# Optimization experiments

Measured on AMD Instinct MI355X. Metric: run time of the kernel, lower is better.

## Reference

```python
import jax, jax.numpy as jnp
import numpy as np

H = 12
DK = 64


def setup_inputs() -> dict:
    key = jax.random.key(0)
    ks = jax.random.split(key, 6)
    bs, ne, d = 32, 20, H * DK
    R = jax.random.normal(ks[0], (bs, ne, ne, d), dtype=jnp.float32)
    R_mas = jax.random.randint(ks[1], (bs, ne, ne, 1), 0, 2).astype(jnp.float32)
    WQ_w = jax.random.normal(ks[2], (DK, DK), dtype=jnp.float32) * (1.0 / np.sqrt(DK))
    WK_w = jax.random.normal(ks[3], (DK, DK), dtype=jnp.float32) * (1.0 / np.sqrt(DK))
    WV_w = jax.random.normal(ks[4], (DK, DK), dtype=jnp.float32) * (1.0 / np.sqrt(DK))
    zb = jnp.zeros((DK,), dtype=jnp.float32)
    return {"R": R, "R_mas": R_mas, "WQ_w": WQ_w, "WQ_b": zb, "WK_w": WK_w,
            "WK_b": zb, "WV_w": WV_w, "WV_b": zb}


def reference(R, R_mas, WQ_w, WQ_b, WK_w, WK_b, WV_w, WV_b):
    bs, ne, _, d = R.shape
    h, dk = H, DK
    n = ne * ne
    # (bs, h, ne, ne, dk)
    Rh = R.reshape(bs, ne, ne, h, dk).transpose(0, 3, 1, 2, 4)
    # per-head QKV linears (torch Linear: y = x @ W.T + b)
    Q = (Rh @ WQ_w.T + WQ_b).reshape(bs, h, n, dk)
    K = (Rh @ WK_w.T + WK_b).reshape(bs, h, n, dk)
    V = (Rh @ WV_w.T + WV_b).reshape(bs, h, n, dk)
    mas = R_mas.reshape(bs, 1, n)                      # (bs,1,n)
    att_mas = mas[:, :, :, None] * mas[:, :, None, :]  # (bs,1,n,n)
    alpha = jnp.einsum('bhqd,bhkd->bhqk', Q, K)        # (bs,h,n,n)
    alpha = alpha - (1.0 - att_mas) * 100000.0         # mask BEFORE scaling (faithful)
    alpha = jax.nn.softmax(alpha / jnp.sqrt(jnp.float32(dk)), axis=-1)
    R_Z = jnp.einsum('bhqk,bhkd->bhqd', alpha, V).reshape(bs, h, ne, ne, dk)
    R_Z = R_Z * R_mas.reshape(bs, 1, ne, ne, 1)
    # (bs, ne, ne, h*dk)
    return R_Z.transpose(0, 2, 3, 1, 4).reshape(bs, ne, ne, h * dk)
```

## Files before the change

### kernel.cpp

```cpp
#include <hip/hip_runtime.h>

typedef float    f32x4 __attribute__((ext_vector_type(4)));
typedef _Float16 f16x8 __attribute__((ext_vector_type(8)));
typedef _Float16 f16x4 __attribute__((ext_vector_type(4)));
typedef _Float16 f16x2 __attribute__((ext_vector_type(2)));
typedef __fp16   fp16x2_raw __attribute__((ext_vector_type(2)));

#define MFMA16 __builtin_amdgcn_mfma_f32_16x16x32_f16

__device__ __forceinline__ f16x2 pkrtz(float a, float b) {
    fp16x2_raw t = __builtin_amdgcn_cvt_pkrtz(a, b);
    union { fp16x2_raw r; f16x2 h; } u;
    u.r = t;
    return u.h;
}
#define PKRTZ pkrtz

#define NQ     400
#define DMODEL 768

#define SCL 0.18033688011112042f
#define PEN 18033.688011112043f
#define M0  8.0f

#define K_OFF    0
#define VT_OFF   51200
#define W_OFF    105472
#define PEN_OFF  130048
#define BIAS_OFF 131648
#define MKB_OFF  132416
#define SMEM_BYTES 132480

__device__ __forceinline__ f16x8 cvt8(const float* rp) {
    f32x4 u0 = *(const f32x4*)(rp);
    f32x4 u1 = *(const f32x4*)(rp + 4);
    union { f16x2 h2[4]; f16x8 v; } u;
    u.h2[0] = PKRTZ(u0[0], u0[1]);
    u.h2[1] = PKRTZ(u0[2], u0[3]);
    u.h2[2] = PKRTZ(u1[0], u1[1]);
    u.h2[3] = PKRTZ(u1[2], u1[3]);
    return u.v;
}

__device__ __forceinline__ void proj_v(char* smem, f16x8 af0, f16x8 af1,
                                       int t, int g, int q16, int csw) {
    #pragma unroll
    for (int cg = 0; cg < 4; ++cg) {
        const int col = cg * 16 + q16;
        const float bb = *(const float*)(smem + BIAS_OFF + (128 + col) * 4);
        f32x4 acc = {bb, bb, bb, bb};
        f16x8 wb0 = *(const f16x8*)(smem + W_OFF + 16384 + col * 128 + ((g * 16) ^ csw));
        f16x8 wb1 = *(const f16x8*)(smem + W_OFF + 16384 + col * 128 + ((64 + g * 16) ^ csw));
        acc = MFMA16(af0, wb0, acc, 0, 0, 0);
        acc = MFMA16(af1, wb1, acc, 0, 0, 0);
        union { f16x2 h2[2]; f16x4 v; } hv;
        hv.h2[0] = PKRTZ(acc[0], acc[1]);
        hv.h2[1] = PKRTZ(acc[2], acc[3]);
        *(f16x4*)(smem + VT_OFF + col * 848 + (t >> 1) * 64 + g * 16 + (t & 1) * 8) = hv.v;
    }
}

__device__ __forceinline__ void proj_k(char* smem, f16x8 af0, f16x8 af1,
                                       int kk, int g, int q16, int csw) {
    #pragma unroll
    for (int cg = 0; cg < 4; ++cg) {
        const int d0 = cg * 16 + 4 * g;
        f32x4 acc = *(const f32x4*)(smem + BIAS_OFF + (64 + d0) * 4);
        f16x8 wb0 = *(const f16x8*)(smem + W_OFF + 8192 + (cg * 16 + q16) * 128 + ((g * 16) ^ csw));
        f16x8 wb1 = *(const f16x8*)(smem + W_OFF + 8192 + (cg * 16 + q16) * 128 + ((64 + g * 16) ^ csw));
        acc = MFMA16(wb0, af0, acc, 0, 0, 0);
        acc = MFMA16(wb1, af1, acc, 0, 0, 0);
        union { f16x2 h2[2]; f16x4 v; } hv;
        hv.h2[0] = PKRTZ(acc[0], acc[1]);
        hv.h2[1] = PKRTZ(acc[2], acc[3]);
        const int pos2 = ((cg & 2) << 5) + g * 16 + (cg & 1) * 8;
        *(f16x4*)(smem + K_OFF + kk * 128 + (pos2 ^ csw)) = hv.v;
    }
}

__device__ __forceinline__ void proj_q(char* smem, f16x8 af0, f16x8 af1,
                                       int g, int q16, int csw, f16x8 (&qreg)[2]) {
    f32x4 qa[4];
    #pragma unroll
    for (int cg = 0; cg < 4; ++cg) {
        const int d0 = cg * 16 + 4 * g;
        f32x4 acc = *(const f32x4*)(smem + BIAS_OFF + d0 * 4);
        f16x8 wb0 = *(const f16x8*)(smem + W_OFF + (cg * 16 + q16) * 128 + ((g * 16) ^ csw));
        f16x8 wb1 = *(const f16x8*)(smem + W_OFF + (cg * 16 + q16) * 128 + ((64 + g * 16) ^ csw));
        acc = MFMA16(wb0, af0, acc, 0, 0, 0);
        acc = MFMA16(wb1, af1, acc, 0, 0, 0);
        qa[cg] = acc;
    }
    union { f16x2 h2[4]; f16x8 v; } u0, u1;
    u0.h2[0] = PKRTZ(qa[0][0], qa[0][1]);
    u0.h2[1] = PKRTZ(qa[0][2], qa[0][3]);
    u0.h2[2] = PKRTZ(qa[1][0], qa[1][1]);
    u0.h2[3] = PKRTZ(qa[1][2], qa[1][3]);
    u1.h2[0] = PKRTZ(qa[2][0], qa[2][1]);
    u1.h2[1] = PKRTZ(qa[2][2], qa[2][3]);
    u1.h2[2] = PKRTZ(qa[3][0], qa[3][1]);
    u1.h2[3] = PKRTZ(qa[3][2], qa[3][3]);
    qreg[0] = u0.v;
    qreg[1] = u1.v;
}

__global__ __launch_bounds__(1024, 4)
void attn_fused(const float* __restrict__ R, const float* __restrict__ Rmas,
                const float* __restrict__ Wq, const float* __restrict__ bq,
                const float* __restrict__ Wk, const float* __restrict__ bk,
                const float* __restrict__ Wv, const float* __restrict__ bv,
                float* __restrict__ out)
{
    extern __shared__ char smem[];
    const int tid  = threadIdx.x;
    const int lane = tid & 63;
    const int wv   = tid >> 6;
    const int g    = lane >> 4;
    const int q16  = lane & 15;
    const int csw  = (q16 & 7) << 4;

    const int blk = blockIdx.x;
    const int b   = blk / 12;
    const int h   = blk % 12;

    {
        if (tid < 768) {
            const int m   = tid >> 8;
            const int idx = tid & 255;
            const int row = idx >> 2;
            const int c0  = (idx & 3) << 4;
            const float* Wm = (m == 0 ? Wq : (m == 1 ? Wk : Wv)) + row * 64 + c0;
            const int sw = (row & 7) << 4;
            #pragma unroll
            for (int k2 = 0; k2 < 2; ++k2) {
                f32x4 v0 = *(const f32x4*)(Wm + 8 * k2);
                f32x4 v1 = *(const f32x4*)(Wm + 8 * k2 + 4);
                union { f16x2 h2[4]; f16x8 v; } hv;
                hv.h2[0] = PKRTZ(v0[0], v0[1]);
                hv.h2[1] = PKRTZ(v0[2], v0[3]);
                hv.h2[2] = PKRTZ(v1[0], v1[1]);
                hv.h2[3] = PKRTZ(v1[2], v1[3]);
                *(f16x8*)(smem + W_OFF + m * 8192 + row * 128 + ((c0 * 2 + 16 * k2) ^ sw)) = hv.v;
            }
        } else if (tid < 960) {
            const int j = tid - 768;
            const float* bms[3] = {bq, bk, bv};
            *(float*)(smem + BIAS_OFF + j * 4) = bms[j >> 6][j & 63];
        }
        if (wv < 7) {
            const int i = (wv << 6) | lane;
            const float mval = (i < NQ) ? Rmas[b * NQ + i] : 0.0f;
            unsigned long long bb = __ballot(mval != 0.0f);
            if (lane == 0) {
                ((unsigned*)(smem + MKB_OFF))[2 * wv]     = (unsigned)bb;
                ((unsigned*)(smem + MKB_OFF))[2 * wv + 1] = (unsigned)(bb >> 32);
            }
        }
        if (tid < 256) {
            const int r = tid >> 2, c = tid & 3;
            *(f16x4*)(smem + VT_OFF + r * 848 + 768 + c * 16 + 8) = (f16x4){0, 0, 0, 0};
        }
    }
    __syncthreads();

    const float* Rbh = R + (size_t)b * NQ * DMODEL + h * 64;

    f16x8 qreg0[2], qreg1[2];
    int qt0 = -1, qt1 = -1;
    #pragma unroll
    for (int i = 0; i < 2; ++i) {
        const int t = wv + 16 * i;
        if (t < 25) {
            const float* rp = Rbh + (size_t)(t * 16 + q16) * DMODEL + g * 8;
            f16x8 af0 = cvt8(rp);
            f16x8 af1 = cvt8(rp + 32);
            proj_k(smem, af0, af1, t * 16 + q16, g, q16, csw);
            proj_v(smem, af0, af1, t, g, q16, csw);
        }
    }
    {
        const int t0 = 2 * wv;
        if (t0 < 25) {
            const float* rp = Rbh + (size_t)(t0 * 16 + q16) * DMODEL + g * 8;
            f16x8 af0 = cvt8(rp);
            f16x8 af1 = cvt8(rp + 32);
            proj_q(smem, af0, af1, g, q16, csw, qreg0);
            qt0 = t0;
        }
        const int t1 = 2 * wv + 1;
        if (t1 < 25) {
            const float* rp = Rbh + (size_t)(t1 * 16 + q16) * DMODEL + g * 8;
            f16x8 af0 = cvt8(rp);
            f16x8 af1 = cvt8(rp + 32);
            proj_q(smem, af0, af1, g, q16, csw, qreg1);
            qt1 = t1;
        }
    }
    if (wv == 15) {
        #pragma unroll
        for (int i = 0; i < 7; ++i) {
            const int k = i * 64 + lane;
            if (k < NQ) {
                const unsigned bit =
                    (((const unsigned*)(smem + MKB_OFF))[k >> 5] >> (k & 31)) & 1u;
                *(float*)(smem + PEN_OFF + k * 4) = bit ? -M0 : -(M0 + PEN);
            }
        }
    }
    __syncthreads();

    if (qt0 >= 0) {
        const bool has2 = (qt1 >= 0);
        const int qrow0 = qt0 * 16 + q16;
        const unsigned qb0 = (((const unsigned*)(smem + MKB_OFF))[qrow0 >> 5] >> (qrow0 & 31)) & 1u;
        const int qrow1 = (has2 ? qt1 : qt0) * 16 + q16;
        const unsigned qb1 = (((const unsigned*)(smem + MKB_OFF))[qrow1 >> 5] >> (qrow1 & 31)) & 1u;

        const int kbase = K_OFF + q16 * 128;
        const int o0 = (g * 16) ^ csw;
        const int o1 = (64 + g * 16) ^ csw;

        f32x4 oc0[4], oc1[4];
        #pragma unroll
        for (int cg = 0; cg < 4; ++cg) {
            oc0[cg] = (f32x4){0.f, 0.f, 0.f, 0.f};
            oc1[cg] = (f32x4){0.f, 0.f, 0.f, 0.f};
        }
        float ps0 = 0.f, ps1 = 0.f;

        f16x8 ka0 = *(const f16x8*)(smem + kbase + o0);
        f16x8 ka1 = *(const f16x8*)(smem + kbase + o1);
        f16x8 kb0 = *(const f16x8*)(smem + kbase + 2048 + o0);
        f16x8 kb1 = *(const f16x8*)(smem + kbase + 2048 + o1);

        #pragma unroll 1
        for (int kc = 0; kc < 12; ++kc) {
            f32x4 pa4 = *(const f32x4*)(smem + PEN_OFF + (kc * 32 + 4 * g) * 4);
            f32x4 pb4 = *(const f32x4*)(smem + PEN_OFF + (kc * 32 + 16 + 4 * g) * 4);

            __builtin_amdgcn_s_setprio(1);
            f32x4 accA0 = {0.f, 0.f, 0.f, 0.f};
            accA0 = MFMA16(ka0, qreg0[0], accA0, 0, 0, 0);
            accA0 = MFMA16(ka1, qreg0[1], accA0, 0, 0, 0);
            f32x4 accB0 = {0.f, 0.f, 0.f, 0.f};
            accB0 = MFMA16(kb0, qreg0[0], accB0, 0, 0, 0);
            accB0 = MFMA16(kb1, qreg0[1], accB0, 0, 0, 0);
            f32x4 accA1 = {0.f, 0.f, 0.f, 0.f};
            f32x4 accB1 = {0.f, 0.f, 0.f, 0.f};
            if (has2) {
                accA1 = MFMA16(ka0, qreg1[0], accA1, 0, 0, 0);
                accA1 = MFMA16(ka1, qreg1[1], accA1, 0, 0, 0);
                accB1 = MFMA16(kb0, qreg1[0], accB1, 0, 0, 0);
                accB1 = MFMA16(kb1, qreg1[1], accB1, 0, 0, 0);
            }
            __builtin_amdgcn_s_setprio(0);

            const char* kn = smem + kbase + (kc + 1) * 4096;
            ka0 = *(const f16x8*)(kn + o0);
            ka1 = *(const f16x8*)(kn + o1);
            kb0 = *(const f16x8*)(kn + 2048 + o0);
            kb1 = *(const f16x8*)(kn + 2048 + o1);

            const float e0 = __builtin_amdgcn_exp2f(fmaf(accA0[0], SCL, pa4[0]));
            const float e1 = __builtin_amdgcn_exp2f(fmaf(accA0[1], SCL, pa4[1]));
            const float e2 = __builtin_amdgcn_exp2f(fmaf(accA0[2], SCL, pa4[2]));
            const float e3 = __builtin_amdgcn_exp2f(fmaf(accA0[3], SCL, pa4[3]));
            const float e4 = __builtin_amdgcn_exp2f(fmaf(accB0[0], SCL, pb4[0]));
            const float e5 = __builtin_amdgcn_exp2f(fmaf(accB0[1], SCL, pb4[1]));
            const float e6 = __builtin_amdgcn_exp2f(fmaf(accB0[2], SCL, pb4[2]));
            const float e7 = __builtin_amdgcn_exp2f(fmaf(accB0[3], SCL, pb4[3]));
            ps0 += ((e0 + e1) + (e2 + e3)) + ((e4 + e5) + (e6 + e7));
            union { f16x2 h2[4]; f16x8 v; } pu0;
            pu0.h2[0] = PKRTZ(e0, e1);
            pu0.h2[1] = PKRTZ(e2, e3);
            pu0.h2[2] = PKRTZ(e4, e5);
            pu0.h2[3] = PKRTZ(e6, e7);
            const f16x8 pfrag0 = pu0.v;

            f16x8 pfrag1;
            if (has2) {
                const float f0 = __builtin_amdgcn_exp2f(fmaf(accA1[0], SCL, pa4[0]));
                const float f1 = __builtin_amdgcn_exp2f(fmaf(accA1[1], SCL, pa4[1]));
                const float f2 = __builtin_amdgcn_exp2f(fmaf(accA1[2], SCL, pa4[2]));
                const float f3 = __builtin_amdgcn_exp2f(fmaf(accA1[3], SCL, pa4[3]));
                const float f4 = __builtin_amdgcn_exp2f(fmaf(accB1[0], SCL, pb4[0]));
                const float f5 = __builtin_amdgcn_exp2f(fmaf(accB1[1], SCL, pb4[1]));
                const float f6 = __builtin_amdgcn_exp2f(fmaf(accB1[2], SCL, pb4[2]));
                const float f7 = __builtin_amdgcn_exp2f(fmaf(accB1[3], SCL, pb4[3]));
                ps1 += ((f0 + f1) + (f2 + f3)) + ((f4 + f5) + (f6 + f7));
                union { f16x2 h2[4]; f16x8 v; } pu1;
                pu1.h2[0] = PKRTZ(f0, f1);
                pu1.h2[1] = PKRTZ(f2, f3);
                pu1.h2[2] = PKRTZ(f4, f5);
                pu1.h2[3] = PKRTZ(f6, f7);
                pfrag1 = pu1.v;
            }

            __builtin_amdgcn_s_setprio(1);
            #pragma unroll
            for (int cg = 0; cg < 4; ++cg) {
                f16x8 vb = *(const f16x8*)(smem + VT_OFF + (cg * 16 + q16) * 848 + kc * 64 + g * 16);
                oc0[cg] = MFMA16(pfrag0, vb, oc0[cg], 0, 0, 0);
                if (has2) oc1[cg] = MFMA16(pfrag1, vb, oc1[cg], 0, 0, 0);
            }
            __builtin_amdgcn_s_setprio(0);
        }
        {
            f32x4 pa4 = *(const f32x4*)(smem + PEN_OFF + (384 + 4 * g) * 4);
            f32x4 accA0 = {0.f, 0.f, 0.f, 0.f};
            accA0 = MFMA16(ka0, qreg0[0], accA0, 0, 0, 0);
            accA0 = MFMA16(ka1, qreg0[1], accA0, 0, 0, 0);
            const float e0 = __builtin_amdgcn_exp2f(fmaf(accA0[0], SCL, pa4[0]));
            const float e1 = __builtin_amdgcn_exp2f(fmaf(accA0[1], SCL, pa4[1]));
            const float e2 = __builtin_amdgcn_exp2f(fmaf(accA0[2], SCL, pa4[2]));
            const float e3 = __builtin_amdgcn_exp2f(fmaf(accA0[3], SCL, pa4[3]));
            ps0 += (e0 + e1) + (e2 + e3);
            union { f16x2 h2[4]; f16x8 v; } pu0;
            pu0.h2[0] = PKRTZ(e0, e1);
            pu0.h2[1] = PKRTZ(e2, e3);
            pu0.h2[2] = (f16x2){0, 0};
            pu0.h2[3] = (f16x2){0, 0};
            const f16x8 pfrag0 = pu0.v;

            f16x8 pfrag1;
            if (has2) {
                f32x4 accA1 = {0.f, 0.f, 0.f, 0.f};
                accA1 = MFMA16(ka0, qreg1[0], accA1, 0, 0, 0);
                accA1 = MFMA16(ka1, qreg1[1], accA1, 0, 0, 0);
                const float f0 = __builtin_amdgcn_exp2f(fmaf(accA1[0], SCL, pa4[0]));
                const float f1 = __builtin_amdgcn_exp2f(fmaf(accA1[1], SCL, pa4[1]));
                const float f2 = __builtin_amdgcn_exp2f(fmaf(accA1[2], SCL, pa4[2]));
                const float f3 = __builtin_amdgcn_exp2f(fmaf(accA1[3], SCL, pa4[3]));
                ps1 += (f0 + f1) + (f2 + f3);
                union { f16x2 h2[4]; f16x8 v; } pu1;
                pu1.h2[0] = PKRTZ(f0, f1);
                pu1.h2[1] = PKRTZ(f2, f3);
                pu1.h2[2] = (f16x2){0, 0};
                pu1.h2[3] = (f16x2){0, 0};
                pfrag1 = pu1.v;
            }
            #pragma unroll
            for (int cg = 0; cg < 4; ++cg) {
                f16x8 vb = *(const f16x8*)(smem + VT_OFF + (cg * 16 + q16) * 848 + 12 * 64 + g * 16);
                oc0[cg] = MFMA16(pfrag0, vb, oc0[cg], 0, 0, 0);
                if (has2) oc1[cg] = MFMA16(pfrag1, vb, oc1[cg], 0, 0, 0);
            }
        }

        ps0 += __shfl_xor(ps0, 16);
        ps0 += __shfl_xor(ps0, 32);
        const float myrs0 = qb0 ? __builtin_amdgcn_rcpf(ps0) : 0.0f;
        float rs[4];
        #pragma unroll
        for (int r = 0; r < 4; ++r) rs[r] = __shfl(myrs0, 4 * g + r);
        float* op0 = out + (size_t)(b * NQ + qt0 * 16) * DMODEL + h * 64;
        #pragma unroll
        for (int r = 0; r < 4; ++r) {
            #pragma unroll
            for (int cg = 0; cg < 4; ++cg)
                op0[(4 * g + r) * DMODEL + cg * 16 + q16] = oc0[cg][r] * rs[r];
        }
        if (has2) {
            ps1 += __shfl_xor(ps1, 16);
            ps1 += __shfl_xor(ps1, 32);
            const float myrs1 = qb1 ? __builtin_amdgcn_rcpf(ps1) : 0.0f;
            #pragma unroll
            for (int r = 0; r < 4; ++r) rs[r] = __shfl(myrs1, 4 * g + r);
            float* op1 = out + (size_t)(b * NQ + qt1 * 16) * DMODEL + h * 64;
            #pragma unroll
            for (int r = 0; r < 4; ++r) {
                #pragma unroll
                for (int cg = 0; cg < 4; ++cg)
                    op1[(4 * g + r) * DMODEL + cg * 16 + q16] = oc1[cg][r] * rs[r];
            }
        }
    }
}

extern "C" void kernel_launch(void* const* d_in, const int* in_sizes, int n_in,
                              void* d_out, int out_size, void* d_ws, size_t ws_size,
                              hipStream_t stream) {
    const float* R    = (const float*)d_in[0];
    const float* Rmas = (const float*)d_in[1];
    const float* Wq   = (const float*)d_in[2];
    const float* bq   = (const float*)d_in[3];
    const float* Wk   = (const float*)d_in[4];
    const float* bk   = (const float*)d_in[5];
    const float* Wv   = (const float*)d_in[6];
    const float* bv   = (const float*)d_in[7];
    float* out = (float*)d_out;

    (void)hipFuncSetAttribute(reinterpret_cast<const void*>(attn_fused),
                              hipFuncAttributeMaxDynamicSharedMemorySize, SMEM_BYTES);
    attn_fused<<<dim3(384), dim3(1024), SMEM_BYTES, stream>>>(R, Rmas, Wq, bq, Wk, bk, Wv, bv, out);
}
```

Baseline: 45.26 us.

## Rebalance grid to 256 blocks, each doing one full head plus half a head

The kernel now launches 256 blocks (8 per batch) instead of 384 (one per batch-head). Each block processes one full head and then half of a second head's query tiles, reusing the shared weights and mask setup. The aim is to match the block count to the GPU's 256 compute units so there is no partial second wave. The cost is that K/V projection for the split heads is recomputed by both blocks that share them, plus an extra barrier between the two segments.

```diff
diff --git a/kernel.cpp b/kernel.cpp
--- a/kernel.cpp
+++ b/kernel.cpp
@@ -120,8 +120,11 @@
     const int csw  = (q16 & 7) << 4;
 
     const int blk = blockIdx.x;
-    const int b   = blk / 12;
-    const int h   = blk % 12;
+    const int b   = blk >> 3;
+    const int j   = blk & 7;
+    int h_full, h_half, qlo2, nt2;
+    if (j & 1) { h_half = (3 * j - 1) >> 1; qlo2 = 13; nt2 = 12; h_full = (3 * j + 1) >> 1; }
+    else       { h_full = (3 * j) >> 1;     h_half = h_full + 1; qlo2 = 0;  nt2 = 13; }
 
     {
         if (tid < 768) {
@@ -143,9 +146,9 @@
                 *(f16x8*)(smem + W_OFF + m * 8192 + row * 128 + ((c0 * 2 + 16 * k2) ^ sw)) = hv.v;
             }
         } else if (tid < 960) {
-            const int j = tid - 768;
+            const int jj = tid - 768;
             const float* bms[3] = {bq, bk, bv};
-            *(float*)(smem + BIAS_OFF + j * 4) = bms[j >> 6][j & 63];
+            *(float*)(smem + BIAS_OFF + jj * 4) = bms[jj >> 6][jj & 63];
         }
         if (wv < 7) {
             const int i = (wv << 6) | lane;
@@ -163,215 +166,224 @@
     }
     __syncthreads();
 
-    const float* Rbh = R + (size_t)b * NQ * DMODEL + h * 64;
-
-    f16x8 qreg0[2], qreg1[2];
-    int qt0 = -1, qt1 = -1;
-    #pragma unroll
-    for (int i = 0; i < 2; ++i) {
-        const int t = wv + 16 * i;
-        if (t < 25) {
+    #pragma unroll 1
+    for (int seg = 0; seg < 2; ++seg) {
+        const int h   = seg ? h_half : h_full;
+        const int qlo = seg ? qlo2 : 0;
+        const int nt  = seg ? nt2  : 25;
+        const float* Rbh = R + (size_t)b * NQ * DMODEL + h * 64;
+
+        if (seg) __syncthreads();
+
+        f16x8 qreg0[2], qreg1[2];
+        const int qt0 = (wv < nt)      ? (qlo + wv)      : -1;
+        const int qt1 = (wv + 16 < nt) ? (qlo + wv + 16) : -1;
+        {
+            const int t = wv;
             const float* rp = Rbh + (size_t)(t * 16 + q16) * DMODEL + g * 8;
             f16x8 af0 = cvt8(rp);
             f16x8 af1 = cvt8(rp + 32);
             proj_k(smem, af0, af1, t * 16 + q16, g, q16, csw);
             proj_v(smem, af0, af1, t, g, q16, csw);
-        }
-    }
-    {
-        const int t0 = 2 * wv;
-        if (t0 < 25) {
-            const float* rp = Rbh + (size_t)(t0 * 16 + q16) * DMODEL + g * 8;
+            if (qt0 == t) proj_q(smem, af0, af1, g, q16, csw, qreg0);
+        }
+        if (wv >= 7) {
+            const int t = wv + 9;
+            const float* rp = Rbh + (size_t)(t * 16 + q16) * DMODEL + g * 8;
+            f16x8 af0 = cvt8(rp);
+            f16x8 af1 = cvt8(rp + 32);
+            proj_k(smem, af0, af1, t * 16 + q16, g, q16, csw);
+            proj_v(smem, af0, af1, t, g, q16, csw);
+        }
+        if (qt0 >= 0 && qt0 != wv) {
+            const float* rp = Rbh + (size_t)(qt0 * 16 + q16) * DMODEL + g * 8;
             f16x8 af0 = cvt8(rp);
             f16x8 af1 = cvt8(rp + 32);
             proj_q(smem, af0, af1, g, q16, csw, qreg0);
-            qt0 = t0;
-        }
-        const int t1 = 2 * wv + 1;
-        if (t1 < 25) {
-            const float* rp = Rbh + (size_t)(t1 * 16 + q16) * DMODEL + g * 8;
+        }
+        if (qt1 >= 0) {
+            const float* rp = Rbh + (size_t)(qt1 * 16 + q16) * DMODEL + g * 8;
             f16x8 af0 = cvt8(rp);
             f16x8 af1 = cvt8(rp + 32);
             proj_q(smem, af0, af1, g, q16, csw, qreg1);
-            qt1 = t1;
-        }
-    }
-    if (wv == 15) {
-        #pragma unroll
-        for (int i = 0; i < 7; ++i) {
-            const int k = i * 64 + lane;
-            if (k < NQ) {
-                const unsigned bit =
-                    (((const unsigned*)(smem + MKB_OFF))[k >> 5] >> (k & 31)) & 1u;
-                *(float*)(smem + PEN_OFF + k * 4) = bit ? -M0 : -(M0 + PEN);
-            }
-        }
-    }
-    __syncthreads();
-
-    if (qt0 >= 0) {
-        const bool has2 = (qt1 >= 0);
-        const int qrow0 = qt0 * 16 + q16;
-        const unsigned qb0 = (((const unsigned*)(smem + MKB_OFF))[qrow0 >> 5] >> (qrow0 & 31)) & 1u;
-        const int qrow1 = (has2 ? qt1 : qt0) * 16 + q16;
-        const unsigned qb1 = (((const unsigned*)(smem + MKB_OFF))[qrow1 >> 5] >> (qrow1 & 31)) & 1u;
-
-        const int kbase = K_OFF + q16 * 128;
-        const int o0 = (g * 16) ^ csw;
-        const int o1 = (64 + g * 16) ^ csw;
-
-        f32x4 oc0[4], oc1[4];
-        #pragma unroll
-        for (int cg = 0; cg < 4; ++cg) {
-            oc0[cg] = (f32x4){0.f, 0.f, 0.f, 0.f};
-            oc1[cg] = (f32x4){0.f, 0.f, 0.f, 0.f};
-        }
-        float ps0 = 0.f, ps1 = 0.f;
-
-        f16x8 ka0 = *(const f16x8*)(smem + kbase + o0);
-        f16x8 ka1 = *(const f16x8*)(smem + kbase + o1);
-        f16x8 kb0 = *(const f16x8*)(smem + kbase + 2048 + o0);
-        f16x8 kb1 = *(const f16x8*)(smem + kbase + 2048 + o1);
-
-        #pragma unroll 1
-        for (int kc = 0; kc < 12; ++kc) {
-            f32x4 pa4 = *(const f32x4*)(smem + PEN_OFF + (kc * 32 + 4 * g) * 4);
-            f32x4 pb4 = *(const f32x4*)(smem + PEN_OFF + (kc * 32 + 16 + 4 * g) * 4);
-
-            __builtin_amdgcn_s_setprio(1);
-            f32x4 accA0 = {0.f, 0.f, 0.f, 0.f};
-            accA0 = MFMA16(ka0, qreg0[0], accA0, 0, 0, 0);
-            accA0 = MFMA16(ka1, qreg0[1], accA0, 0, 0, 0);
-            f32x4 accB0 = {0.f, 0.f, 0.f, 0.f};
-            accB0 = MFMA16(kb0, qreg0[0], accB0, 0, 0, 0);
-            accB0 = MFMA16(kb1, qreg0[1], accB0, 0, 0, 0);
-            f32x4 accA1 = {0.f, 0.f, 0.f, 0.f};
-            f32x4 accB1 = {0.f, 0.f, 0.f, 0.f};
-            if (has2) {
-                accA1 = MFMA16(ka0, qreg1[0], accA1, 0, 0, 0);
-                accA1 = MFMA16(ka1, qreg1[1], accA1, 0, 0, 0);
-                accB1 = MFMA16(kb0, qreg1[0], accB1, 0, 0, 0);
-                accB1 = MFMA16(kb1, qreg1[1], accB1, 0, 0, 0);
-            }
-            __builtin_amdgcn_s_setprio(0);
-
-            const char* kn = smem + kbase + (kc + 1) * 4096;
-            ka0 = *(const f16x8*)(kn + o0);
-            ka1 = *(const f16x8*)(kn + o1);
-            kb0 = *(const f16x8*)(kn + 2048 + o0);
-            kb1 = *(const f16x8*)(kn + 2048 + o1);
-
-            const float e0 = __builtin_amdgcn_exp2f(fmaf(accA0[0], SCL, pa4[0]));
-            const float e1 = __builtin_amdgcn_exp2f(fmaf(accA0[1], SCL, pa4[1]));
-            const float e2 = __builtin_amdgcn_exp2f(fmaf(accA0[2], SCL, pa4[2]));
-            const float e3 = __builtin_amdgcn_exp2f(fmaf(accA0[3], SCL, pa4[3]));
-            const float e4 = __builtin_amdgcn_exp2f(fmaf(accB0[0], SCL, pb4[0]));
-            const float e5 = __builtin_amdgcn_exp2f(fmaf(accB0[1], SCL, pb4[1]));
-            const float e6 = __builtin_amdgcn_exp2f(fmaf(accB0[2], SCL, pb4[2]));
-            const float e7 = __builtin_amdgcn_exp2f(fmaf(accB0[3], SCL, pb4[3]));
-            ps0 += ((e0 + e1) + (e2 + e3)) + ((e4 + e5) + (e6 + e7));
-            union { f16x2 h2[4]; f16x8 v; } pu0;
-            pu0.h2[0] = PKRTZ(e0, e1);
-            pu0.h2[1] = PKRTZ(e2, e3);
-            pu0.h2[2] = PKRTZ(e4, e5);
-            pu0.h2[3] = PKRTZ(e6, e7);
-            const f16x8 pfrag0 = pu0.v;
-
-            f16x8 pfrag1;
-            if (has2) {
-                const float f0 = __builtin_amdgcn_exp2f(fmaf(accA1[0], SCL, pa4[0]));
-                const float f1 = __builtin_amdgcn_exp2f(fmaf(accA1[1], SCL, pa4[1]));
-                const float f2 = __builtin_amdgcn_exp2f(fmaf(accA1[2], SCL, pa4[2]));
-                const float f3 = __builtin_amdgcn_exp2f(fmaf(accA1[3], SCL, pa4[3]));
-                const float f4 = __builtin_amdgcn_exp2f(fmaf(accB1[0], SCL, pb4[0]));
-                const float f5 = __builtin_amdgcn_exp2f(fmaf(accB1[1], SCL, pb4[1]));
-                const float f6 = __builtin_amdgcn_exp2f(fmaf(accB1[2], SCL, pb4[2]));
-                const float f7 = __builtin_amdgcn_exp2f(fmaf(accB1[3], SCL, pb4[3]));
-                ps1 += ((f0 + f1) + (f2 + f3)) + ((f4 + f5) + (f6 + f7));
-                union { f16x2 h2[4]; f16x8 v; } pu1;
-                pu1.h2[0] = PKRTZ(f0, f1);
-                pu1.h2[1] = PKRTZ(f2, f3);
-                pu1.h2[2] = PKRTZ(f4, f5);
-                pu1.h2[3] = PKRTZ(f6, f7);
-                pfrag1 = pu1.v;
-            }
-
-            __builtin_amdgcn_s_setprio(1);
+        }
+        if (seg == 0 && wv == 15) {
+            #pragma unroll
+            for (int i = 0; i < 7; ++i) {
+                const int k = i * 64 + lane;
+                if (k < NQ) {
+                    const unsigned bit =
+                        (((const unsigned*)(smem + MKB_OFF))[k >> 5] >> (k & 31)) & 1u;
+                    *(float*)(smem + PEN_OFF + k * 4) = bit ? -M0 : -(M0 + PEN);
+                }
+            }
+        }
+        __syncthreads();
+
+        if (qt0 >= 0) {
+            const bool has2 = (qt1 >= 0);
+            const int qrow0 = qt0 * 16 + q16;
+            const unsigned qb0 = (((const unsigned*)(smem + MKB_OFF))[qrow0 >> 5] >> (qrow0 & 31)) & 1u;
+            const int qrow1 = (has2 ? qt1 : qt0) * 16 + q16;
+            const unsigned qb1 = (((const unsigned*)(smem + MKB_OFF))[qrow1 >> 5] >> (qrow1 & 31)) & 1u;
+
+            const int kbase = K_OFF + q16 * 128;
+            const int o0 = (g * 16) ^ csw;
+            const int o1 = (64 + g * 16) ^ csw;
+
+            f32x4 oc0[4], oc1[4];
             #pragma unroll
             for (int cg = 0; cg < 4; ++cg) {
-                f16x8 vb = *(const f16x8*)(smem + VT_OFF + (cg * 16 + q16) * 848 + kc * 64 + g * 16);
-                oc0[cg] = MFMA16(pfrag0, vb, oc0[cg], 0, 0, 0);
-                if (has2) oc1[cg] = MFMA16(pfrag1, vb, oc1[cg], 0, 0, 0);
-            }
-            __builtin_amdgcn_s_setprio(0);
-        }
-        {
-            f32x4 pa4 = *(const f32x4*)(smem + PEN_OFF + (384 + 4 * g) * 4);
-            f32x4 accA0 = {0.f, 0.f, 0.f, 0.f};
-            accA0 = MFMA16(ka0, qreg0[0], accA0, 0, 0, 0);
-            accA0 = MFMA16(ka1, qreg0[1], accA0, 0, 0, 0);
-            const float e0 = __builtin_amdgcn_exp2f(fmaf(accA0[0], SCL, pa4[0]));
-            const float e1 = __builtin_amdgcn_exp2f(fmaf(accA0[1], SCL, pa4[1]));
-            const float e2 = __builtin_amdgcn_exp2f(fmaf(accA0[2], SCL, pa4[2]));
-            const float e3 = __builtin_amdgcn_exp2f(fmaf(accA0[3], SCL, pa4[3]));
-            ps0 += (e0 + e1) + (e2 + e3);
-            union { f16x2 h2[4]; f16x8 v; } pu0;
-            pu0.h2[0] = PKRTZ(e0, e1);
-            pu0.h2[1] = PKRTZ(e2, e3);
-            pu0.h2[2] = (f16x2){0, 0};
-            pu0.h2[3] = (f16x2){0, 0};
-            const f16x8 pfrag0 = pu0.v;
-
-            f16x8 pfrag1;
-            if (has2) {
+                oc0[cg] = (f32x4){0.f, 0.f, 0.f, 0.f};
+                oc1[cg] = (f32x4){0.f, 0.f, 0.f, 0.f};
+            }
+            float ps0 = 0.f, ps1 = 0.f;
+
+            f16x8 ka0 = *(const f16x8*)(smem + kbase + o0);
+            f16x8 ka1 = *(const f16x8*)(smem + kbase + o1);
+            f16x8 kb0 = *(const f16x8*)(smem + kbase + 2048 + o0);
+            f16x8 kb1 = *(const f16x8*)(smem + kbase + 2048 + o1);
+
+            #pragma unroll 1
+            for (int kc = 0; kc < 12; ++kc) {
+                f32x4 pa4 = *(const f32x4*)(smem + PEN_OFF + (kc * 32 + 4 * g) * 4);
+                f32x4 pb4 = *(const f32x4*)(smem + PEN_OFF + (kc * 32 + 16 + 4 * g) * 4);
+
+                __builtin_amdgcn_s_setprio(1);
+                f32x4 accA0 = {0.f, 0.f, 0.f, 0.f};
+                accA0 = MFMA16(ka0, qreg0[0], accA0, 0, 0, 0);
+                accA0 = MFMA16(ka1, qreg0[1], accA0, 0, 0, 0);
+                f32x4 accB0 = {0.f, 0.f, 0.f, 0.f};
+                accB0 = MFMA16(kb0, qreg0[0], accB0, 0, 0, 0);
+                accB0 = MFMA16(kb1, qreg0[1], accB0, 0, 0, 0);
                 f32x4 accA1 = {0.f, 0.f, 0.f, 0.f};
-                accA1 = MFMA16(ka0, qreg1[0], accA1, 0, 0, 0);
-                accA1 = MFMA16(ka1, qreg1[1], accA1, 0, 0, 0);
-                const float f0 = __builtin_amdgcn_exp2f(fmaf(accA1[0], SCL, pa4[0]));
-                const float f1 = __builtin_amdgcn_exp2f(fmaf(accA1[1], SCL, pa4[1]));
-                const float f2 = __builtin_amdgcn_exp2f(fmaf(accA1[2], SCL, pa4[2]));
-                const float f3 = __builtin_amdgcn_exp2f(fmaf(accA1[3], SCL, pa4[3]));
-                ps1 += (f0 + f1) + (f2 + f3);
-                union { f16x2 h2[4]; f16x8 v; } pu1;
-                pu1.h2[0] = PKRTZ(f0, f1);
-                pu1.h2[1] = PKRTZ(f2, f3);
-                pu1.h2[2] = (f16x2){0, 0};
-                pu1.h2[3] = (f16x2){0, 0};
-                pfrag1 = pu1.v;
-            }
+                f32x4 accB1 = {0.f, 0.f, 0.f, 0.f};
+                if (has2) {
+                    accA1 = MFMA16(ka0, qreg1[0], accA1, 0, 0, 0);
+                    accA1 = MFMA16(ka1, qreg1[1], accA1, 0, 0, 0);
+                    accB1 = MFMA16(kb0, qreg1[0], accB1, 0, 0, 0);
+                    accB1 = MFMA16(kb1, qreg1[1], accB1, 0, 0, 0);
+                }
+                __builtin_amdgcn_s_setprio(0);
+
+                const char* kn = smem + kbase + (kc + 1) * 4096;
+                ka0 = *(const f16x8*)(kn + o0);
+                ka1 = *(const f16x8*)(kn + o1);
+                kb0 = *(const f16x8*)(kn + 2048 + o0);
+                kb1 = *(const f16x8*)(kn + 2048 + o1);
+
+                const float e0 = __builtin_amdgcn_exp2f(fmaf(accA0[0], SCL, pa4[0]));
+                const float e1 = __builtin_amdgcn_exp2f(fmaf(accA0[1], SCL, pa4[1]));
+                const float e2 = __builtin_amdgcn_exp2f(fmaf(accA0[2], SCL, pa4[2]));
+                const float e3 = __builtin_amdgcn_exp2f(fmaf(accA0[3], SCL, pa4[3]));
+                const float e4 = __builtin_amdgcn_exp2f(fmaf(accB0[0], SCL, pb4[0]));
+                const float e5 = __builtin_amdgcn_exp2f(fmaf(accB0[1], SCL, pb4[1]));
+                const float e6 = __builtin_amdgcn_exp2f(fmaf(accB0[2], SCL, pb4[2]));
+                const float e7 = __builtin_amdgcn_exp2f(fmaf(accB0[3], SCL, pb4[3]));
+                ps0 += ((e0 + e1) + (e2 + e3)) + ((e4 + e5) + (e6 + e7));
+                union { f16x2 h2[4]; f16x8 v; } pu0;
+                pu0.h2[0] = PKRTZ(e0, e1);
+                pu0.h2[1] = PKRTZ(e2, e3);
+                pu0.h2[2] = PKRTZ(e4, e5);
+                pu0.h2[3] = PKRTZ(e6, e7);
+                const f16x8 pfrag0 = pu0.v;
+
+                f16x8 pfrag1;
+                if (has2) {
+                    const float f0 = __builtin_amdgcn_exp2f(fmaf(accA1[0], SCL, pa4[0]));
+                    const float f1 = __builtin_amdgcn_exp2f(fmaf(accA1[1], SCL, pa4[1]));
+                    const float f2 = __builtin_amdgcn_exp2f(fmaf(accA1[2], SCL, pa4[2]));
+                    const float f3 = __builtin_amdgcn_exp2f(fmaf(accA1[3], SCL, pa4[3]));
+                    const float f4 = __builtin_amdgcn_exp2f(fmaf(accB1[0], SCL, pb4[0]));
+                    const float f5 = __builtin_amdgcn_exp2f(fmaf(accB1[1], SCL, pb4[1]));
+                    const float f6 = __builtin_amdgcn_exp2f(fmaf(accB1[2], SCL, pb4[2]));
+                    const float f7 = __builtin_amdgcn_exp2f(fmaf(accB1[3], SCL, pb4[3]));
+                    ps1 += ((f0 + f1) + (f2 + f3)) + ((f4 + f5) + (f6 + f7));
+                    union { f16x2 h2[4]; f16x8 v; } pu1;
+                    pu1.h2[0] = PKRTZ(f0, f1);
+                    pu1.h2[1] = PKRTZ(f2, f3);
+                    pu1.h2[2] = PKRTZ(f4, f5);
+                    pu1.h2[3] = PKRTZ(f6, f7);
+                    pfrag1 = pu1.v;
+                }
+
+                __builtin_amdgcn_s_setprio(1);
+                #pragma unroll
+                for (int cg = 0; cg < 4; ++cg) {
+                    f16x8 vb = *(const f16x8*)(smem + VT_OFF + (cg * 16 + q16) * 848 + kc * 64 + g * 16);
+                    oc0[cg] = MFMA16(pfrag0, vb, oc0[cg], 0, 0, 0);
+                    if (has2) oc1[cg] = MFMA16(pfrag1, vb, oc1[cg], 0, 0, 0);
+                }
+                __builtin_amdgcn_s_setprio(0);
+            }
+            {
+                f32x4 pa4 = *(const f32x4*)(smem + PEN_OFF + (384 + 4 * g) * 4);
+                f32x4 accA0 = {0.f, 0.f, 0.f, 0.f};
+                accA0 = MFMA16(ka0, qreg0[0], accA0, 0, 0, 0);
+                accA0 = MFMA16(ka1, qreg0[1], accA0, 0, 0, 0);
+                const float e0 = __builtin_amdgcn_exp2f(fmaf(accA0[0], SCL, pa4[0]));
+                const float e1 = __builtin_amdgcn_exp2f(fmaf(accA0[1], SCL, pa4[1]));
+                const float e2 = __builtin_amdgcn_exp2f(fmaf(accA0[2], SCL, pa4[2]));
+                const float e3 = __builtin_amdgcn_exp2f(fmaf(accA0[3], SCL, pa4[3]));
+                ps0 += (e0 + e1) + (e2 + e3);
+                union { f16x2 h2[4]; f16x8 v; } pu0;
+                pu0.h2[0] = PKRTZ(e0, e1);
+                pu0.h2[1] = PKRTZ(e2, e3);
+                pu0.h2[2] = (f16x2){0, 0};
+                pu0.h2[3] = (f16x2){0, 0};
+                const f16x8 pfrag0 = pu0.v;
+
+                f16x8 pfrag1;
+                if (has2) {
+                    f32x4 accA1 = {0.f, 0.f, 0.f, 0.f};
+                    accA1 = MFMA16(ka0, qreg1[0], accA1, 0, 0, 0);
+                    accA1 = MFMA16(ka1, qreg1[1], accA1, 0, 0, 0);
+                    const float f0 = __builtin_amdgcn_exp2f(fmaf(accA1[0], SCL, pa4[0]));
+                    const float f1 = __builtin_amdgcn_exp2f(fmaf(accA1[1], SCL, pa4[1]));
+                    const float f2 = __builtin_amdgcn_exp2f(fmaf(accA1[2], SCL, pa4[2]));
+                    const float f3 = __builtin_amdgcn_exp2f(fmaf(accA1[3], SCL, pa4[3]));
+                    ps1 += (f0 + f1) + (f2 + f3);
+                    union { f16x2 h2[4]; f16x8 v; } pu1;
+                    pu1.h2[0] = PKRTZ(f0, f1);
+                    pu1.h2[1] = PKRTZ(f2, f3);
+                    pu1.h2[2] = (f16x2){0, 0};
+                    pu1.h2[3] = (f16x2){0, 0};
+                    pfrag1 = pu1.v;
+                }
+                #pragma unroll
+                for (int cg = 0; cg < 4; ++cg) {
+                    f16x8 vb = *(const f16x8*)(smem + VT_OFF + (cg * 16 + q16) * 848 + 12 * 64 + g * 16);
+                    oc0[cg] = MFMA16(pfrag0, vb, oc0[cg], 0, 0, 0);
+                    if (has2) oc1[cg] = MFMA16(pfrag1, vb, oc1[cg], 0, 0, 0);
+                }
+            }
+
+            ps0 += __shfl_xor(ps0, 16);
+            ps0 += __shfl_xor(ps0, 32);
+            const float myrs0 = qb0 ? __builtin_amdgcn_rcpf(ps0) : 0.0f;
+            float rs[4];
             #pragma unroll
-            for (int cg = 0; cg < 4; ++cg) {
-                f16x8 vb = *(const f16x8*)(smem + VT_OFF + (cg * 16 + q16) * 848 + 12 * 64 + g * 16);
-                oc0[cg] = MFMA16(pfrag0, vb, oc0[cg], 0, 0, 0);
-                if (has2) oc1[cg] = MFMA16(pfrag1, vb, oc1[cg], 0, 0, 0);
-            }
-        }
-
-        ps0 += __shfl_xor(ps0, 16);
-        ps0 += __shfl_xor(ps0, 32);
-        const float myrs0 = qb0 ? __builtin_amdgcn_rcpf(ps0) : 0.0f;
-        float rs[4];
-        #pragma unroll
-        for (int r = 0; r < 4; ++r) rs[r] = __shfl(myrs0, 4 * g + r);
-        float* op0 = out + (size_t)(b * NQ + qt0 * 16) * DMODEL + h * 64;
-        #pragma unroll
-        for (int r = 0; r < 4; ++r) {
-            #pragma unroll
-            for (int cg = 0; cg < 4; ++cg)
-                op0[(4 * g + r) * DMODEL + cg * 16 + q16] = oc0[cg][r] * rs[r];
-        }
-        if (has2) {
-            ps1 += __shfl_xor(ps1, 16);
-            ps1 += __shfl_xor(ps1, 32);
-            const float myrs1 = qb1 ? __builtin_amdgcn_rcpf(ps1) : 0.0f;
-            #pragma unroll
-            for (int r = 0; r < 4; ++r) rs[r] = __shfl(myrs1, 4 * g + r);
-            float* op1 = out + (size_t)(b * NQ + qt1 * 16) * DMODEL + h * 64;
+            for (int r = 0; r < 4; ++r) rs[r] = __shfl(myrs0, 4 * g + r);
+            float* op0 = out + (size_t)(b * NQ + qt0 * 16) * DMODEL + h * 64;
             #pragma unroll
             for (int r = 0; r < 4; ++r) {
                 #pragma unroll
                 for (int cg = 0; cg < 4; ++cg)
-                    op1[(4 * g + r) * DMODEL + cg * 16 + q16] = oc1[cg][r] * rs[r];
+                    op0[(4 * g + r) * DMODEL + cg * 16 + q16] = oc0[cg][r] * rs[r];
+            }
+            if (has2) {
+                ps1 += __shfl_xor(ps1, 16);
+                ps1 += __shfl_xor(ps1, 32);
+                const float myrs1 = qb1 ? __builtin_amdgcn_rcpf(ps1) : 0.0f;
+                #pragma unroll
+                for (int r = 0; r < 4; ++r) rs[r] = __shfl(myrs1, 4 * g + r);
+                float* op1 = out + (size_t)(b * NQ + qt1 * 16) * DMODEL + h * 64;
+                #pragma unroll
+                for (int r = 0; r < 4; ++r) {
+                    #pragma unroll
+                    for (int cg = 0; cg < 4; ++cg)
+                        op1[(4 * g + r) * DMODEL + cg * 16 + q16] = oc1[cg][r] * rs[r];
+                }
             }
         }
     }
@@ -392,5 +404,5 @@
 
     (void)hipFuncSetAttribute(reinterpret_cast<const void*>(attn_fused),
                               hipFuncAttributeMaxDynamicSharedMemorySize, SMEM_BYTES);
-    attn_fused<<<dim3(384), dim3(1024), SMEM_BYTES, stream>>>(R, Rmas, Wq, bq, Wk, bk, Wv, bv, out);
-}
+    attn_fused<<<dim3(256), dim3(1024), SMEM_BYTES, stream>>>(R, Rmas, Wq, bq, Wk, bk, Wv, bv, out);
+}
```

Result: slower. 79.59 us (+75.9%).
